# Kernel optimization log

Measured on AMD Instinct MI355X. Metric: run time of the kernel, lower is better.

The kernel has to match this reference:

```python
import jax, jax.numpy as jnp
import numpy as np

R, T, N, D = 16, 512, 256, 22  # runs, timesteps, agents, sensing dim


def setup_inputs() -> dict:
    key = jax.random.key(0)
    k_runs, k_comm, k_w1, k_b1, k_w2, k_b2 = jax.random.split(key, 6)
    runs = jax.random.normal(k_runs, (R, T, N, D), dtype=jnp.float32)
    # comm vector per run has length N+2 with zero sentinels at both ends
    comm0 = jax.random.uniform(k_comm, (R, N + 2), dtype=jnp.float32)
    W1 = jax.random.normal(k_w1, (D + 2, 22), dtype=jnp.float32) * 0.2
    b1 = jax.random.normal(k_b1, (22,), dtype=jnp.float32) * 0.1
    W2 = jax.random.normal(k_w2, (22, 2), dtype=jnp.float32) * 0.2
    b2 = jax.random.normal(k_b2, (2,), dtype=jnp.float32) * 0.1
    return {"runs": runs, "comm0": comm0, "W1": W1, "b1": b1, "W2": W2, "b2": b2}


def reference(runs, comm0, W1, b1, W2, b2):
    # zero the sentinel endpoints (init_comm puts 0.0 at both ends)
    comm0 = comm0.at[:, 0].set(0.0).at[:, -1].set(0.0)

    def agent_step(comm, ix):
        # comm: [N+2]; sequential update: agent i reads comm[i] (left, already
        # updated this timestep) and comm[i+2] (right, stale), writes comm[i+1].
        i, x = ix
        left = jax.lax.dynamic_slice(comm, (i,), (1,))
        right = jax.lax.dynamic_slice(comm, (i + 2,), (1,))
        inp = jnp.concatenate([x, left, right])            # [D+2]
        h = jnp.tanh(inp @ W1 + b1)                        # [22]
        out = h @ W2 + b2                                  # [2]
        comm = jax.lax.dynamic_update_slice(
            comm, jax.nn.sigmoid(out[1])[None], (i + 1,))
        return comm, out[0]                                # control (raw speed)

    def time_step(comm, xs):
        # xs: [N, D]
        comm, controls = jax.lax.scan(agent_step, comm, (jnp.arange(N), xs))
        return comm, controls                              # controls: [N]

    def run_fn(c0, run):
        # run: [T, N, D]
        _, controls = jax.lax.scan(time_step, c0, run)
        return controls                                    # [T, N]

    return jax.vmap(run_fn)(comm0, runs)                   # [R, T, N]
```

## Files before the change

kernel.cpp:

```cpp
#include <hip/hip_runtime.h>

#define R_ 16
#define T_ 512
#define N_ 256
#define D_ 22
#define DTOT 1278

constexpr float TWO_LOG2E = 2.8853900817779268f;
constexpr float LOG2E     = 1.4426950408889634f;

__global__ __launch_bounds__(256) void pre_kernel(const float* __restrict__ runs,
                                                  const float* __restrict__ W1,
                                                  const float* __restrict__ b1,
                                                  float* __restrict__ pre) {
    __shared__ float sx[256 * 23];
    const size_t base = (size_t)blockIdx.x * (256 * 22);

    for (int m = threadIdx.x; m < 256 * 22; m += 256) {
        int row = m / 22;
        int k = m - row * 22;
        sx[row * 23 + k] = runs[base + m];
    }
    __syncthreads();

    float x[22];
#pragma unroll
    for (int k = 0; k < 22; ++k) x[k] = sx[threadIdx.x * 23 + k];

    float acc[22];
#pragma unroll
    for (int j = 0; j < 22; ++j) acc[j] = b1[j];
#pragma unroll
    for (int k = 0; k < 22; ++k) {
#pragma unroll
        for (int j = 0; j < 22; ++j)
            acc[j] = fmaf(x[k], W1[k * 22 + j], acc[j]);
    }
#pragma unroll
    for (int j = 0; j < 22; ++j) sx[threadIdx.x * 23 + j] = acc[j] * TWO_LOG2E;
    __syncthreads();

    for (int m = threadIdx.x; m < 256 * 22; m += 256) {
        int row = m / 22;
        int k = m - row * 22;
        pre[base + m] = sx[row * 23 + k];
    }
}

__global__ __launch_bounds__(512, 1) void wave_kernel(const float* __restrict__ pre,
                                                      const float* __restrict__ comm0,
                                                      const float* __restrict__ W1,
                                                      const float* __restrict__ W2,
                                                      const float* __restrict__ b2,
                                                      float* __restrict__ out) {
    __shared__ float comm[N_ + 2];
    const int tid = threadIdx.x;
    const int r = blockIdx.x;
    const int sidx = tid >> 2;
    const int l = tid & 3;
    const int jb = l * 6;

    if (tid < N_ + 2)
        comm[tid] = (tid == 0 || tid == N_ + 1) ? 0.f : comm0[r * (N_ + 2) + tid];

    float A2[6], B2[6], Wa[6], Wb[6];
#pragma unroll
    for (int q = 0; q < 6; ++q) {
        int j = jb + q;
        bool jv = (j < 22);
        A2[q] = jv ? W1[484 + j] * TWO_LOG2E : 0.f;
        B2[q] = jv ? W1[506 + j] * TWO_LOG2E : 0.f;
        Wa[q] = jv ? W2[2 * j] : 0.f;
        Wb[q] = jv ? W2[2 * j + 1] : 0.f;
    }
    const float bb0 = b2[0], bb1 = b2[1];
    const float* preR = pre + (size_t)r * ((size_t)T_ * N_ * 22);
    float* outR = out + (size_t)r * ((size_t)T_ * N_);
    __syncthreads();

    const int q2i = (jb + 4 <= 20) ? ((jb >> 1) + 2) : 10;

    float pA[6], pB[6], pC[6];

    auto PF = [&](float* buf, int d) {
        int tl = (d > 255) ? ((d - 254) >> 1) : 0;
        int t = tl + sidx;
        int i = d - 2 * t;
        bool v = (t < T_) && (i >= 0) && (d < DTOT);
        size_t row = v ? ((size_t)t * N_ + i) : 0;
        const float2* p = reinterpret_cast<const float2*>(preR + row * 22);
        float2 a = p[jb >> 1];
        float2 b = p[(jb >> 1) + 1];
        float2 c = p[q2i];
        buf[0] = a.x; buf[1] = a.y; buf[2] = b.x;
        buf[3] = b.y; buf[4] = c.x; buf[5] = c.y;
    };

    auto ST = [&](int d, float* buf) {
        int tl = (d > 255) ? ((d - 254) >> 1) : 0;
        int t = tl + sidx;
        int i = d - 2 * t;
        bool v = (t < T_) && (i >= 0);
        float left = 0.f, right = 0.f;
        if (v) { left = comm[i]; right = comm[i + 2]; }
        float a0 = 0.f, a1 = 0.f;
#pragma unroll
        for (int q = 0; q < 6; ++q) {
            float u = fmaf(right, B2[q], fmaf(left, A2[q], buf[q]));
            float e = __builtin_amdgcn_exp2f(u);
            float h = fmaf(-2.f, __builtin_amdgcn_rcpf(1.f + e), 1.f);
            a0 = fmaf(h, Wa[q], a0);
            a1 = fmaf(h, Wb[q], a1);
        }
        a0 += __shfl_xor(a0, 1); a1 += __shfl_xor(a1, 1);
        a0 += __shfl_xor(a0, 2); a1 += __shfl_xor(a1, 2);
        if (v && l == 0) {
            outR[(size_t)t * N_ + i] = a0 + bb0;
            float o1 = a1 + bb1;
            comm[i + 1] = __builtin_amdgcn_rcpf(
                1.f + __builtin_amdgcn_exp2f(-LOG2E * o1));
        }
    };

#define BAR() do { asm volatile("s_waitcnt lgkmcnt(0)" ::: "memory"); \
                   __builtin_amdgcn_s_barrier();                      \
                   asm volatile("" ::: "memory"); } while (0)

    PF(pA, 0);
    PF(pB, 1);
    for (int d = 0; d < DTOT; d += 3) {
        PF(pC, d + 2); ST(d,     pA); BAR();
        PF(pA, d + 3); ST(d + 1, pB); BAR();
        PF(pB, d + 4); ST(d + 2, pC); BAR();
    }
#undef BAR
}

extern "C" void kernel_launch(void* const* d_in, const int* in_sizes, int n_in,
                              void* d_out, int out_size, void* d_ws, size_t ws_size,
                              hipStream_t stream) {
    const float* runs  = (const float*)d_in[0];
    const float* comm0 = (const float*)d_in[1];
    const float* W1    = (const float*)d_in[2];
    const float* b1    = (const float*)d_in[3];
    const float* W2    = (const float*)d_in[4];
    const float* b2    = (const float*)d_in[5];
    float* out = (float*)d_out;

    const size_t preBytes = (size_t)R_ * T_ * N_ * 22 * sizeof(float);
    float* pre = (ws_size >= preBytes) ? (float*)d_ws : (float*)d_in[0];

    pre_kernel<<<(R_ * T_ * N_) / 256, 256, 0, stream>>>(runs, W1, b1, pre);
    wave_kernel<<<R_, 512, 0, stream>>>(pre, comm0, W1, W2, b2, out);
}
```

Measured before the change: 1.065 ms.

## Pack two runs per block, halve lanes per agent, and move control output off the critical path

The wave kernel now handles two runs per 512-thread block, using 2 lanes per agent with 12 hidden units each instead of 4 lanes with 6. The lane reduction uses a DPP xor-1 swap instead of two shuffles. The speed output (a0) is computed after the barrier, so only the comm-producing path sits on the serial dependency chain. The pre-kernel also gets vectorized float4 loads and stores and caches pre-scaled weights in LDS. The trade-off is that each block runs more work per diagonal step and the grid drops to 8 blocks, which lowers device-level parallelism.

```diff
diff --git a/kernel.cpp b/kernel.cpp
--- a/kernel.cpp
+++ b/kernel.cpp
@@ -3,7 +3,6 @@
 #define R_ 16
 #define T_ 512
 #define N_ 256
-#define D_ 22
 #define DTOT 1278
 
 constexpr float TWO_LOG2E = 2.8853900817779268f;
@@ -13,38 +12,46 @@
                                                   const float* __restrict__ W1,
                                                   const float* __restrict__ b1,
                                                   float* __restrict__ pre) {
-    __shared__ float sx[256 * 23];
-    const size_t base = (size_t)blockIdx.x * (256 * 22);
+    __shared__ float4 sx4[1408];
+    __shared__ float sw[506];
+    float* sx = (float*)sx4;
 
-    for (int m = threadIdx.x; m < 256 * 22; m += 256) {
-        int row = m / 22;
-        int k = m - row * 22;
-        sx[row * 23 + k] = runs[base + m];
-    }
+    for (int m = threadIdx.x; m < 506; m += 256)
+        sw[m] = (m < 484 ? W1[m] : b1[m - 484]) * TWO_LOG2E;
+
+    const float4* rin = (const float4*)(runs + (size_t)blockIdx.x * 5632);
+    for (int m = threadIdx.x; m < 1408; m += 256) sx4[m] = rin[m];
     __syncthreads();
 
     float x[22];
+    const float2* rowp = (const float2*)(sx + threadIdx.x * 22);
 #pragma unroll
-    for (int k = 0; k < 22; ++k) x[k] = sx[threadIdx.x * 23 + k];
+    for (int p = 0; p < 11; ++p) { float2 w = rowp[p]; x[2*p] = w.x; x[2*p+1] = w.y; }
 
     float acc[22];
 #pragma unroll
-    for (int j = 0; j < 22; ++j) acc[j] = b1[j];
+    for (int j = 0; j < 22; ++j) acc[j] = sw[484 + j];
 #pragma unroll
     for (int k = 0; k < 22; ++k) {
+        float xk = x[k];
+        const float* wr = &sw[k * 22];
 #pragma unroll
-        for (int j = 0; j < 22; ++j)
-            acc[j] = fmaf(x[k], W1[k * 22 + j], acc[j]);
+        for (int j = 0; j < 22; ++j) acc[j] = fmaf(xk, wr[j], acc[j]);
     }
+    __syncthreads();
+    float2* roww = (float2*)(sx + threadIdx.x * 22);
 #pragma unroll
-    for (int j = 0; j < 22; ++j) sx[threadIdx.x * 23 + j] = acc[j] * TWO_LOG2E;
+    for (int p = 0; p < 11; ++p) roww[p] = make_float2(acc[2*p], acc[2*p+1]);
     __syncthreads();
 
-    for (int m = threadIdx.x; m < 256 * 22; m += 256) {
-        int row = m / 22;
-        int k = m - row * 22;
-        pre[base + m] = sx[row * 23 + k];
-    }
+    float4* pout = (float4*)(pre + (size_t)blockIdx.x * 5632);
+    for (int m = threadIdx.x; m < 1408; m += 256) pout[m] = sx4[m];
+}
+
+__device__ __forceinline__ float dpp_xor1(float x) {
+    int i = __builtin_bit_cast(int, x);
+    i = __builtin_amdgcn_update_dpp(0, i, 0xB1, 0xF, 0xF, true);
+    return __builtin_bit_cast(float, i);
 }
 
 __global__ __launch_bounds__(512, 1) void wave_kernel(const float* __restrict__ pre,
@@ -53,19 +60,25 @@
                                                       const float* __restrict__ W2,
                                                       const float* __restrict__ b2,
                                                       float* __restrict__ out) {
-    __shared__ float comm[N_ + 2];
+    __shared__ float comm[2][N_ + 2];
     const int tid = threadIdx.x;
-    const int r = blockIdx.x;
-    const int sidx = tid >> 2;
-    const int l = tid & 3;
-    const int jb = l * 6;
+    const int rsel = tid >> 8;
+    const int ltid = tid & 255;
+    const int r = 2 * blockIdx.x + rsel;
+    const int sidx = ltid >> 1;
+    const int l = ltid & 1;
+    const int jb = l * 12;
 
-    if (tid < N_ + 2)
-        comm[tid] = (tid == 0 || tid == N_ + 1) ? 0.f : comm0[r * (N_ + 2) + tid];
+    for (int m = tid; m < 2 * (N_ + 2); m += 512) {
+        int q = m / (N_ + 2), p = m - q * (N_ + 2);
+        comm[q][p] = (p == 0 || p == N_ + 1)
+                         ? 0.f
+                         : comm0[(2 * blockIdx.x + q) * (N_ + 2) + p];
+    }
 
-    float A2[6], B2[6], Wa[6], Wb[6];
+    float A2[12], B2[12], Wa[12], Wb[12];
 #pragma unroll
-    for (int q = 0; q < 6; ++q) {
+    for (int q = 0; q < 12; ++q) {
         int j = jb + q;
         bool jv = (j < 22);
         A2[q] = jv ? W1[484 + j] * TWO_LOG2E : 0.f;
@@ -76,50 +89,61 @@
     const float bb0 = b2[0], bb1 = b2[1];
     const float* preR = pre + (size_t)r * ((size_t)T_ * N_ * 22);
     float* outR = out + (size_t)r * ((size_t)T_ * N_);
+    float* commS = comm[rsel];
     __syncthreads();
 
-    const int q2i = (jb + 4 <= 20) ? ((jb >> 1) + 2) : 10;
+    const int f2b = l * 6;
 
-    float pA[6], pB[6], pC[6];
+    float pA[12], pB[12], pC[12], h[12];
 
     auto PF = [&](float* buf, int d) {
         int tl = (d > 255) ? ((d - 254) >> 1) : 0;
         int t = tl + sidx;
         int i = d - 2 * t;
-        bool v = (t < T_) && (i >= 0) && (d < DTOT);
+        bool v = (t < T_) && (i >= 0);
         size_t row = v ? ((size_t)t * N_ + i) : 0;
         const float2* p = reinterpret_cast<const float2*>(preR + row * 22);
-        float2 a = p[jb >> 1];
-        float2 b = p[(jb >> 1) + 1];
-        float2 c = p[q2i];
-        buf[0] = a.x; buf[1] = a.y; buf[2] = b.x;
-        buf[3] = b.y; buf[4] = c.x; buf[5] = c.y;
+#pragma unroll
+        for (int q = 0; q < 6; ++q) {
+            int fi = f2b + q; if (fi > 10) fi = 10;
+            float2 w = p[fi];
+            buf[2 * q] = w.x; buf[2 * q + 1] = w.y;
+        }
     };
 
-    auto ST = [&](int d, float* buf) {
+    auto ST1 = [&](int d, float* buf) {
         int tl = (d > 255) ? ((d - 254) >> 1) : 0;
         int t = tl + sidx;
         int i = d - 2 * t;
         bool v = (t < T_) && (i >= 0);
-        float left = 0.f, right = 0.f;
-        if (v) { left = comm[i]; right = comm[i + 2]; }
-        float a0 = 0.f, a1 = 0.f;
+        int iu = i < 0 ? 0 : (i > 255 ? 255 : i);
+        float left = commS[iu], right = commS[iu + 2];
+        float a1 = 0.f;
 #pragma unroll
-        for (int q = 0; q < 6; ++q) {
+        for (int q = 0; q < 12; ++q) {
             float u = fmaf(right, B2[q], fmaf(left, A2[q], buf[q]));
             float e = __builtin_amdgcn_exp2f(u);
-            float h = fmaf(-2.f, __builtin_amdgcn_rcpf(1.f + e), 1.f);
-            a0 = fmaf(h, Wa[q], a0);
-            a1 = fmaf(h, Wb[q], a1);
+            h[q] = fmaf(-2.f, __builtin_amdgcn_rcpf(1.f + e), 1.f);
+            a1 = fmaf(h[q], Wb[q], a1);
         }
-        a0 += __shfl_xor(a0, 1); a1 += __shfl_xor(a1, 1);
-        a0 += __shfl_xor(a0, 2); a1 += __shfl_xor(a1, 2);
+        a1 += dpp_xor1(a1);
         if (v && l == 0) {
-            outR[(size_t)t * N_ + i] = a0 + bb0;
             float o1 = a1 + bb1;
-            comm[i + 1] = __builtin_amdgcn_rcpf(
+            commS[i + 1] = __builtin_amdgcn_rcpf(
                 1.f + __builtin_amdgcn_exp2f(-LOG2E * o1));
         }
+    };
+
+    auto ST2 = [&](int d) {
+        int tl = (d > 255) ? ((d - 254) >> 1) : 0;
+        int t = tl + sidx;
+        int i = d - 2 * t;
+        bool v = (t < T_) && (i >= 0);
+        float a0 = 0.f;
+#pragma unroll
+        for (int q = 0; q < 12; ++q) a0 = fmaf(h[q], Wa[q], a0);
+        a0 += dpp_xor1(a0);
+        if (v && l == 0) outR[(size_t)t * N_ + i] = a0 + bb0;
     };
 
 #define BAR() do { asm volatile("s_waitcnt lgkmcnt(0)" ::: "memory"); \
@@ -129,9 +153,9 @@
     PF(pA, 0);
     PF(pB, 1);
     for (int d = 0; d < DTOT; d += 3) {
-        PF(pC, d + 2); ST(d,     pA); BAR();
-        PF(pA, d + 3); ST(d + 1, pB); BAR();
-        PF(pB, d + 4); ST(d + 2, pC); BAR();
+        PF(pC, d + 2); ST1(d, pA);     BAR(); ST2(d);
+        PF(pA, d + 3); ST1(d + 1, pB); BAR(); ST2(d + 1);
+        PF(pB, d + 4); ST1(d + 2, pC); BAR(); ST2(d + 2);
     }
 #undef BAR
 }
@@ -151,5 +175,5 @@
     float* pre = (ws_size >= preBytes) ? (float*)d_ws : (float*)d_in[0];
 
     pre_kernel<<<(R_ * T_ * N_) / 256, 256, 0, stream>>>(runs, W1, b1, pre);
-    wave_kernel<<<R_, 512, 0, stream>>>(pre, comm0, W1, W2, b2, out);
+    wave_kernel<<<R_ / 2, 512, 0, stream>>>(pre, comm0, W1, W2, b2, out);
 }
```

Result: slower. 1.990 ms (+86.8%).
